# Kernel optimization log

Hardware: AMD Instinct MI355X
Metric: run time of the kernel (lower is better)

## Reference

```python
import jax, jax.numpy as jnp
import numpy as np

D_MODEL = 1024
N_HEADS = 16
HEAD_DIM = D_MODEL // N_HEADS
D_FF = 4096
LN_EPS = 1e-5


def _layer_norm(x, gamma, beta):
    mu = jnp.mean(x, axis=-1, keepdims=True)
    var = jnp.var(x, axis=-1, keepdims=True)
    return (x - mu) * jax.lax.rsqrt(var + LN_EPS) * gamma + beta


def setup_inputs() -> dict:
    key = jax.random.key(0)
    ks = jax.random.split(key, 16)
    s = 1.0 / np.sqrt(D_MODEL)
    sf = 1.0 / np.sqrt(D_FF)
    return {
        "x": jax.random.normal(ks[0], (4, 2048, D_MODEL), dtype=jnp.float32),
        "w_q": jax.random.uniform(ks[1], (D_MODEL, D_MODEL), jnp.float32, -s, s),
        "b_q": jax.random.uniform(ks[2], (D_MODEL,), jnp.float32, -s, s),
        "w_k": jax.random.uniform(ks[3], (D_MODEL, D_MODEL), jnp.float32, -s, s),
        "b_k": jax.random.uniform(ks[4], (D_MODEL,), jnp.float32, -s, s),
        "w_v": jax.random.uniform(ks[5], (D_MODEL, D_MODEL), jnp.float32, -s, s),
        "b_v": jax.random.uniform(ks[6], (D_MODEL,), jnp.float32, -s, s),
        "w_o": jax.random.uniform(ks[7], (D_MODEL, D_MODEL), jnp.float32, -s, s),
        "b_o": jax.random.uniform(ks[8], (D_MODEL,), jnp.float32, -s, s),
        "ln1_g": jnp.ones((D_MODEL,), jnp.float32),
        "ln1_b": jnp.zeros((D_MODEL,), jnp.float32),
        "w1": jax.random.uniform(ks[9], (D_MODEL, D_FF), jnp.float32, -s, s),
        "b1": jax.random.uniform(ks[10], (D_FF,), jnp.float32, -s, s),
        "w2": jax.random.uniform(ks[11], (D_FF, D_MODEL), jnp.float32, -sf, sf),
        "b2": jax.random.uniform(ks[12], (D_MODEL,), jnp.float32, -sf, sf),
        "ln2_g": jnp.ones((D_MODEL,), jnp.float32),
        "ln2_b": jnp.zeros((D_MODEL,), jnp.float32),
    }


def reference(x, w_q, b_q, w_k, b_k, w_v, b_v, w_o, b_o,
              ln1_g, ln1_b, w1, b1, w2, b2, ln2_g, ln2_b):
    B, S, D = x.shape
    # projections -> [B, H, S, Hd]
    def split_heads(t):
        return t.reshape(B, S, N_HEADS, HEAD_DIM).transpose(0, 2, 1, 3)
    q = split_heads(x @ w_q + b_q)
    k = split_heads(x @ w_k + b_k)
    v = split_heads(x @ w_v + b_v)
    scale = jnp.float32(np.sqrt(HEAD_DIM))
    scores = jnp.einsum('bhqd,bhkd->bhqk', q, k) / scale
    attn = jax.nn.softmax(scores, axis=-1)  # dropout = identity in eval
    ctx = jnp.einsum('bhqk,bhkd->bhqd', attn, v)
    ctx = ctx.transpose(0, 2, 1, 3).reshape(B, S, D)
    attn_out = ctx @ w_o + b_o
    h = _layer_norm(x + attn_out, ln1_g, ln1_b)
    ffn = jax.nn.relu(h @ w1 + b1) @ w2 + b2
    return _layer_norm(h + ffn, ln2_g, ln2_b)
```

## Files before the change

kernel.cpp:

```cpp
#include <hip/hip_runtime.h>
#include <cstdint>
#include <cstddef>

typedef unsigned short u16;
typedef short s16x8 __attribute__((ext_vector_type(8)));
typedef unsigned short u16x8 __attribute__((ext_vector_type(8)));
typedef unsigned short u16x4 __attribute__((ext_vector_type(4)));
typedef float f32x4 __attribute__((ext_vector_type(4)));

#define MFMA_BF16(a, b, c) __builtin_amdgcn_mfma_f32_16x16x32_bf16((a), (b), (c), 0, 0, 0)

__device__ __forceinline__ float b2f(u16 u) {
    union { unsigned int i; float f; } x;
    x.i = ((unsigned int)u) << 16;
    return x.f;
}
__device__ __forceinline__ u16 f2b(float f) {
    union { float f; unsigned int i; } x;
    x.f = f;
    return (u16)((x.i + 0x8000u) >> 16);
}
__device__ __forceinline__ float exp2_hw(float x) {
    float r;
    asm volatile("v_exp_f32 %0, %1" : "=v"(r) : "v"(x));
    return r;
}

__device__ __forceinline__ void gload_lds16(const u16* g, u16* l) {
    __builtin_amdgcn_global_load_lds((__attribute__((address_space(1))) void*)(g),
                                     (__attribute__((address_space(3))) void*)(l),
                                     16, 0, 0);
}

__global__ __launch_bounds__(256)
void cvt_f32_bf16(const float* __restrict__ in, u16* __restrict__ out) {
    const int i = (blockIdx.x * 256 + threadIdx.x) * 8;
    float4 a = *(const float4*)(in + i);
    float4 b = *(const float4*)(in + i + 4);
    u16x8 o;
    o[0] = f2b(a.x); o[1] = f2b(a.y); o[2] = f2b(a.z); o[3] = f2b(a.w);
    o[4] = f2b(b.x); o[5] = f2b(b.y); o[6] = f2b(b.z); o[7] = f2b(b.w);
    *(u16x8*)(out + i) = o;
}

__global__ __launch_bounds__(256)
void transpose_cvt(const float* __restrict__ in, u16* __restrict__ out, int R, int C) {
    __shared__ u16 t[64][68];
    const int tc = blockIdx.x * 64, tr = blockIdx.y * 64;
    for (int i = 0; i < 16; i++) {
        int idx = threadIdx.x + i * 256;
        int r = idx >> 6, c = idx & 63;
        t[r][c] = f2b(in[(size_t)(tr + r) * C + tc + c]);
    }
    __syncthreads();
    for (int i = 0; i < 16; i++) {
        int idx = threadIdx.x + i * 256;
        int r = idx >> 6, c = idx & 63;
        out[(size_t)(tc + r) * R + tr + c] = t[c][r];
    }
}

enum { EPI_PLAIN = 0, EPI_RELU = 1, EPI_QKV = 2 };
#define SC_QK 0.1803368801111204f

template <int EPI>
__global__ __launch_bounds__(256)
void gemm_bt(const u16* __restrict__ A, const u16* __restrict__ Bt,
             const float* __restrict__ bias0, const float* __restrict__ bias1,
             const float* __restrict__ bias2,
             u16* __restrict__ C0, u16* __restrict__ C1, u16* __restrict__ C2,
             int M, int N, int K) {
    __shared__ u16 As[128 * 32];
    __shared__ u16 Bs[128 * 32];
    const int tid = threadIdx.x;
    const int lane = tid & 63;
    const int wave = tid >> 6;
    const int qd = lane >> 4, cl = lane & 15;
    const int wr = (wave >> 1) * 64, wc = (wave & 1) * 64;
    const int m0 = blockIdx.x * 128, n0 = blockIdx.y * 128;

    const int eo0 = tid * 8, eo1 = 2048 + tid * 8;
    const u16* Ag0 = A + (size_t)(m0 + (eo0 >> 5)) * K + (eo0 & 31);
    const u16* Ag1 = A + (size_t)(m0 + (eo1 >> 5)) * K + (eo1 & 31);
    const u16* Bg0 = Bt + (size_t)(n0 + (eo0 >> 5)) * K + (eo0 & 31);
    const u16* Bg1 = Bt + (size_t)(n0 + (eo1 >> 5)) * K + (eo1 & 31);

    const f32x4 Z = {0.f, 0.f, 0.f, 0.f};
    f32x4 acc[4][4];
    for (int i = 0; i < 4; i++)
        for (int j = 0; j < 4; j++) acc[i][j] = Z;

    for (int k = 0; k < K; k += 32) {
        __syncthreads();
        gload_lds16(Ag0 + k, As + eo0);
        gload_lds16(Ag1 + k, As + eo1);
        gload_lds16(Bg0 + k, Bs + eo0);
        gload_lds16(Bg1 + k, Bs + eo1);
        __syncthreads();
        s16x8 af[4], bfr[4];
        for (int i = 0; i < 4; i++)
            af[i] = *(const s16x8*)(As + (wr + i * 16 + cl) * 32 + qd * 8);
        for (int j = 0; j < 4; j++)
            bfr[j] = *(const s16x8*)(Bs + (wc + j * 16 + cl) * 32 + qd * 8);
        for (int i = 0; i < 4; i++)
            for (int j = 0; j < 4; j++)
                acc[i][j] = MFMA_BF16(af[i], bfr[j], acc[i][j]);
    }

    for (int j = 0; j < 4; j++) {
        const int col = n0 + wc + j * 16 + cl;
        float bv;
        if (EPI == EPI_QKV) {
            const int t = col >> 10, nn = col & 1023;
            const float* bp = (t == 0) ? bias0 : ((t == 1) ? bias1 : bias2);
            bv = bp[nn];
        } else {
            bv = bias0[col];
        }
        if (EPI == EPI_QKV && (col >> 10) == 2) {
            const int nn = col & 1023;
            const int hh = nn >> 6, d = nn & 63;
            for (int i = 0; i < 4; i++) {
                const int row0 = m0 + wr + i * 16 + qd * 4;
                const int b = row0 >> 11, s = row0 & 2047;
                const int bh = b * 16 + hh;
                u16x4 pk;
                for (int r = 0; r < 4; r++) pk[r] = f2b(acc[i][j][r] + bv);
                *(u16x4*)(&C2[((size_t)bh * 64 + d) * 2048 + s]) = pk;
            }
        } else {
            for (int i = 0; i < 4; i++) {
                for (int r = 0; r < 4; r++) {
                    const int row = m0 + wr + i * 16 + qd * 4 + r;
                    float v = acc[i][j][r] + bv;
                    if (EPI == EPI_RELU) v = fmaxf(v, 0.f);
                    if (EPI == EPI_QKV) {
                        const int t = col >> 10, nn = col & 1023;
                        const int hh = nn >> 6, d = nn & 63;
                        const int b = row >> 11, s = row & 2047;
                        const int bh = b * 16 + hh;
                        if (t == 0)
                            C0[((size_t)bh * 2048 + s) * 64 + d] = f2b(v * SC_QK);
                        else
                            C1[((size_t)bh * 2048 + s) * 64 + d] = f2b(v);
                    } else {
                        C0[(size_t)row * N + col] = f2b(v);
                    }
                }
            }
        }
    }
}

__global__ __launch_bounds__(256)
void flash_attn(const u16* __restrict__ Q, const u16* __restrict__ K,
                const u16* __restrict__ Vt, u16* __restrict__ ctx) {
    __shared__ u16 Ks[64 * 64];
    __shared__ u16 Vs[64 * 64];
    __shared__ u16 Ps[4][32 * 72];
    const int tid = threadIdx.x, lane = tid & 63, wave = tid >> 6;
    const int qd = lane >> 4, cl = lane & 15;
    const int bh = blockIdx.y;
    const int s0 = blockIdx.x * 128 + wave * 32;

    const u16* Qb = Q + ((size_t)bh * 2048 + s0) * 64;
    s16x8 qf[2][2];
    for (int m = 0; m < 2; m++) {
        qf[m][0] = *(const s16x8*)(Qb + (m * 16 + cl) * 64 + qd * 8);
        qf[m][1] = *(const s16x8*)(Qb + (m * 16 + cl) * 64 + 32 + qd * 8);
    }

    const f32x4 Z = {0.f, 0.f, 0.f, 0.f};
    f32x4 o_acc[2][4], l_lane[2];
    for (int m = 0; m < 2; m++) {
        l_lane[m] = Z;
        for (int t = 0; t < 4; t++) o_acc[m][t] = Z;
    }

    const u16* Kb = K + (size_t)bh * 2048 * 64;
    const u16* Vb = Vt + (size_t)bh * 64 * 2048;

    const int e0 = tid, e1 = tid + 256;
    const int r0 = e0 >> 3, bb0 = (e0 & 7) ^ (r0 & 7);
    const int r1 = e1 >> 3, bb1 = (e1 & 7) ^ (r1 & 7);
    u16* pw = &Ps[wave][0];

    for (int kb = 0; kb < 32; kb++) {
        __syncthreads();
        gload_lds16(Kb + (size_t)(kb * 64 + r0) * 64 + bb0 * 8, Ks + e0 * 8);
        gload_lds16(Kb + (size_t)(kb * 64 + r1) * 64 + bb1 * 8, Ks + e1 * 8);
        gload_lds16(Vb + (size_t)r0 * 2048 + kb * 64 + bb0 * 8, Vs + e0 * 8);
        gload_lds16(Vb + (size_t)r1 * 2048 + kb * 64 + bb1 * 8, Vs + e1 * 8);
        __syncthreads();

        f32x4 sacc[2][4];
        for (int m = 0; m < 2; m++)
            for (int t = 0; t < 4; t++) sacc[m][t] = Z;
        for (int t = 0; t < 4; t++) {
            const int row = t * 16 + cl;
            s16x8 kf0 = *(const s16x8*)(Ks + row * 64 + (qd ^ (row & 7)) * 8);
            s16x8 kf1 = *(const s16x8*)(Ks + row * 64 + ((qd + 4) ^ (row & 7)) * 8);
            for (int m = 0; m < 2; m++) {
                sacc[m][t] = MFMA_BF16(qf[m][0], kf0, sacc[m][t]);
                sacc[m][t] = MFMA_BF16(qf[m][1], kf1, sacc[m][t]);
            }
        }

        for (int m = 0; m < 2; m++)
            for (int t = 0; t < 4; t++) {
                f32x4 p;
                for (int r = 0; r < 4; r++) p[r] = exp2_hw(sacc[m][t][r]);
                l_lane[m] += p;
                for (int r = 0; r < 4; r++)
                    pw[(m * 16 + qd * 4 + r) * 72 + t * 16 + cl] = f2b(p[r]);
            }

        for (int kk = 0; kk < 2; kk++) {
            s16x8 vf[4];
            for (int t = 0; t < 4; t++) {
                const int row = t * 16 + cl;
                vf[t] = *(const s16x8*)(Vs + row * 64 +
                                        ((kk * 4 + qd) ^ (row & 7)) * 8);
            }
            for (int m = 0; m < 2; m++) {
                s16x8 pf = *(const s16x8*)(pw + (m * 16 + cl) * 72 + kk * 32 + qd * 8);
                for (int t = 0; t < 4; t++)
                    o_acc[m][t] = MFMA_BF16(pf, vf[t], o_acc[m][t]);
            }
        }
    }

    const int b = bh >> 4, hh = bh & 15;
    for (int m = 0; m < 2; m++)
        for (int r = 0; r < 4; r++) {
            float l = l_lane[m][r];
            for (int off = 1; off < 16; off <<= 1)
                l += __shfl_xor(l, off, 16);
            const float inv = 1.f / l;
            const int s = s0 + m * 16 + qd * 4 + r;
            for (int t = 0; t < 4; t++)
                ctx[((size_t)(b * 2048 + s)) * 1024 + hh * 64 + t * 16 + cl] =
                    f2b(o_acc[m][t][r] * inv);
        }
}

template <int MODE>
__global__ __launch_bounds__(256)
void ln_res(const void* __restrict__ Xv, const u16* __restrict__ Y,
            const float* __restrict__ G, const float* __restrict__ Bp,
            void* __restrict__ Ov) {
    const int row = blockIdx.x * 4 + (threadIdx.x >> 6);
    const int lane = threadIdx.x & 63;
    const int off = lane * 16;
    float v[16];
    float s = 0.f, s2 = 0.f;
    const u16* y = Y + (size_t)row * 1024 + off;
    if (MODE == 0) {
        const float* X = (const float*)Xv + (size_t)row * 1024 + off;
        for (int i = 0; i < 2; i++) {
            float4 xa = *(const float4*)(X + i * 8);
            float4 xb = *(const float4*)(X + i * 8 + 4);
            u16x8 yv = *(const u16x8*)(y + i * 8);
            float xs[8] = {xa.x, xa.y, xa.z, xa.w, xb.x, xb.y, xb.z, xb.w};
            for (int j = 0; j < 8; j++) {
                const float t = xs[j] + b2f(yv[j]);
                v[i * 8 + j] = t;
                s += t;
                s2 += t * t;
            }
        }
    } else {
        const u16* X = (const u16*)Xv + (size_t)row * 1024 + off;
        for (int i = 0; i < 2; i++) {
            u16x8 xv = *(const u16x8*)(X + i * 8);
            u16x8 yv = *(const u16x8*)(y + i * 8);
            for (int j = 0; j < 8; j++) {
                const float t = b2f(xv[j]) + b2f(yv[j]);
                v[i * 8 + j] = t;
                s += t;
                s2 += t * t;
            }
        }
    }
    for (int o = 32; o >= 1; o >>= 1) {
        s += __shfl_xor(s, o, 64);
        s2 += __shfl_xor(s2, o, 64);
    }
    const float mu = s * (1.f / 1024.f);
    const float var = s2 * (1.f / 1024.f) - mu * mu;
    const float rs = rsqrtf(var + 1e-5f);
    const float* g = G + off;
    const float* bp = Bp + off;
    for (int i = 0; i < 2; i++) {
        float4 ga = *(const float4*)(g + i * 8);
        float4 gb = *(const float4*)(g + i * 8 + 4);
        float4 ba = *(const float4*)(bp + i * 8);
        float4 bb = *(const float4*)(bp + i * 8 + 4);
        float gs[8] = {ga.x, ga.y, ga.z, ga.w, gb.x, gb.y, gb.z, gb.w};
        float bs[8] = {ba.x, ba.y, ba.z, ba.w, bb.x, bb.y, bb.z, bb.w};
        if (MODE == 0) {
            u16* o = (u16*)Ov + (size_t)row * 1024 + off;
            u16x8 ov;
            for (int j = 0; j < 8; j++)
                ov[j] = f2b((v[i * 8 + j] - mu) * rs * gs[j] + bs[j]);
            *(u16x8*)(o + i * 8) = ov;
        } else {
            float* o = (float*)Ov + (size_t)row * 1024 + off;
            float4 o0, o1;
            o0.x = (v[i * 8 + 0] - mu) * rs * gs[0] + bs[0];
            o0.y = (v[i * 8 + 1] - mu) * rs * gs[1] + bs[1];
            o0.z = (v[i * 8 + 2] - mu) * rs * gs[2] + bs[2];
            o0.w = (v[i * 8 + 3] - mu) * rs * gs[3] + bs[3];
            o1.x = (v[i * 8 + 4] - mu) * rs * gs[4] + bs[4];
            o1.y = (v[i * 8 + 5] - mu) * rs * gs[5] + bs[5];
            o1.z = (v[i * 8 + 6] - mu) * rs * gs[6] + bs[6];
            o1.w = (v[i * 8 + 7] - mu) * rs * gs[7] + bs[7];
            *(float4*)(o + i * 8) = o0;
            *(float4*)(o + i * 8 + 4) = o1;
        }
    }
}

extern "C" void kernel_launch(void* const* d_in, const int* in_sizes, int n_in,
                              void* d_out, int out_size, void* d_ws, size_t ws_size,
                              hipStream_t stream) {
    const float* x    = (const float*)d_in[0];
    const float* w_q  = (const float*)d_in[1];
    const float* b_q  = (const float*)d_in[2];
    const float* w_k  = (const float*)d_in[3];
    const float* b_k  = (const float*)d_in[4];
    const float* w_v  = (const float*)d_in[5];
    const float* b_v  = (const float*)d_in[6];
    const float* w_o  = (const float*)d_in[7];
    const float* b_o  = (const float*)d_in[8];
    const float* ln1g = (const float*)d_in[9];
    const float* ln1b = (const float*)d_in[10];
    const float* w1   = (const float*)d_in[11];
    const float* b1   = (const float*)d_in[12];
    const float* w2   = (const float*)d_in[13];
    const float* b2   = (const float*)d_in[14];
    const float* ln2g = (const float*)d_in[15];
    const float* ln2b = (const float*)d_in[16];
    float* out = (float*)d_out;

    char* ws = (char*)d_ws;
    const size_t MB = 1024 * 1024;
    u16* wqkv_t = (u16*)(ws + 0);
    u16* wo_t   = (u16*)(ws + 6 * MB);
    u16* w1_t   = (u16*)(ws + 8 * MB);
    u16* w2_t   = (u16*)(ws + 16 * MB);
    u16* x_bf   = (u16*)(ws + 24 * MB);
    u16* Qs     = (u16*)(ws + 40 * MB);
    u16* Kk     = (u16*)(ws + 56 * MB);
    u16* Vt     = (u16*)(ws + 72 * MB);
    u16* ctx    = (u16*)(ws + 88 * MB);
    u16* attn   = (u16*)(ws + 104 * MB);
    u16* h      = attn;
    u16* ffn1   = (u16*)(ws + 24 * MB);
    u16* ffn2   = (u16*)(ws + 88 * MB);

    transpose_cvt<<<dim3(16, 16), 256, 0, stream>>>(w_q, wqkv_t, 1024, 1024);
    transpose_cvt<<<dim3(16, 16), 256, 0, stream>>>(w_k, wqkv_t + 1024 * 1024, 1024, 1024);
    transpose_cvt<<<dim3(16, 16), 256, 0, stream>>>(w_v, wqkv_t + 2 * 1024 * 1024, 1024, 1024);
    transpose_cvt<<<dim3(16, 16), 256, 0, stream>>>(w_o, wo_t, 1024, 1024);
    transpose_cvt<<<dim3(64, 16), 256, 0, stream>>>(w1, w1_t, 1024, 4096);
    transpose_cvt<<<dim3(16, 64), 256, 0, stream>>>(w2, w2_t, 4096, 1024);

    cvt_f32_bf16<<<4096, 256, 0, stream>>>(x, x_bf);

    gemm_bt<EPI_QKV><<<dim3(64, 24), 256, 0, stream>>>(
        x_bf, wqkv_t, b_q, b_k, b_v, Qs, Kk, Vt, 8192, 3072, 1024);

    flash_attn<<<dim3(16, 64), 256, 0, stream>>>(Qs, Kk, Vt, ctx);

    gemm_bt<EPI_PLAIN><<<dim3(64, 8), 256, 0, stream>>>(
        ctx, wo_t, b_o, nullptr, nullptr, attn, nullptr, nullptr, 8192, 1024, 1024);

    ln_res<0><<<2048, 256, 0, stream>>>(x, attn, ln1g, ln1b, h);

    gemm_bt<EPI_RELU><<<dim3(64, 32), 256, 0, stream>>>(
        h, w1_t, b1, nullptr, nullptr, ffn1, nullptr, nullptr, 8192, 4096, 1024);
    gemm_bt<EPI_PLAIN><<<dim3(64, 8), 256, 0, stream>>>(
        ffn1, w2_t, b2, nullptr, nullptr, ffn2, nullptr, nullptr, 8192, 1024, 4096);

    ln_res<1><<<2048, 256, 0, stream>>>(h, ffn2, ln2g, ln2b, out);

    (void)in_sizes; (void)n_in; (void)out_size; (void)ws_size;
}
```

Baseline: 580.8 us.

## Deepen GEMM K-tile to 64 with swizzled LDS; load attention K/V directly to registers

The GEMM now stages a 64-wide K slice per iteration into an XOR-swizzled LDS tile, which halves the number of barrier pairs per output tile and avoids bank conflicts on the fragment reads. The flash attention kernel drops its shared K/V staging and block barriers. Each wave loads its K and V fragments straight from global memory into registers, and the V loads are issued early so they overlap the softmax. In exchange the four waves of a block each fetch the same K/V data on their own, relying on cache for reuse, and register pressure rises.

New measurement: 671.5 us. +15.6%, slower.

```diff
diff --git a/kernel.cpp b/kernel.cpp
--- a/kernel.cpp
+++ b/kernel.cpp
@@ -70,8 +70,8 @@
              const float* __restrict__ bias2,
              u16* __restrict__ C0, u16* __restrict__ C1, u16* __restrict__ C2,
              int M, int N, int K) {
-    __shared__ u16 As[128 * 32];
-    __shared__ u16 Bs[128 * 32];
+    __shared__ u16 As[128 * 64];
+    __shared__ u16 Bs[128 * 64];
     const int tid = threadIdx.x;
     const int lane = tid & 63;
     const int wave = tid >> 6;
@@ -79,32 +79,46 @@
     const int wr = (wave >> 1) * 64, wc = (wave & 1) * 64;
     const int m0 = blockIdx.x * 128, n0 = blockIdx.y * 128;
 
-    const int eo0 = tid * 8, eo1 = 2048 + tid * 8;
-    const u16* Ag0 = A + (size_t)(m0 + (eo0 >> 5)) * K + (eo0 & 31);
-    const u16* Ag1 = A + (size_t)(m0 + (eo1 >> 5)) * K + (eo1 & 31);
-    const u16* Bg0 = Bt + (size_t)(n0 + (eo0 >> 5)) * K + (eo0 & 31);
-    const u16* Bg1 = Bt + (size_t)(n0 + (eo1 >> 5)) * K + (eo1 & 31);
+    const u16* AgP[4];
+    const u16* BgP[4];
+    int dsto[4];
+    for (int c = 0; c < 4; c++) {
+        const int d = tid * 8 + c * 2048;
+        const int row = d >> 6;
+        const int sblk = ((d >> 3) & 7) ^ (row & 7);
+        AgP[c] = A + (size_t)(m0 + row) * K + sblk * 8;
+        BgP[c] = Bt + (size_t)(n0 + row) * K + sblk * 8;
+        dsto[c] = d;
+    }
 
     const f32x4 Z = {0.f, 0.f, 0.f, 0.f};
     f32x4 acc[4][4];
     for (int i = 0; i < 4; i++)
         for (int j = 0; j < 4; j++) acc[i][j] = Z;
 
-    for (int k = 0; k < K; k += 32) {
+    for (int k = 0; k < K; k += 64) {
         __syncthreads();
-        gload_lds16(Ag0 + k, As + eo0);
-        gload_lds16(Ag1 + k, As + eo1);
-        gload_lds16(Bg0 + k, Bs + eo0);
-        gload_lds16(Bg1 + k, Bs + eo1);
+        for (int c = 0; c < 4; c++) {
+            gload_lds16(AgP[c] + k, As + dsto[c]);
+            gload_lds16(BgP[c] + k, Bs + dsto[c]);
+        }
         __syncthreads();
-        s16x8 af[4], bfr[4];
-        for (int i = 0; i < 4; i++)
-            af[i] = *(const s16x8*)(As + (wr + i * 16 + cl) * 32 + qd * 8);
-        for (int j = 0; j < 4; j++)
-            bfr[j] = *(const s16x8*)(Bs + (wc + j * 16 + cl) * 32 + qd * 8);
-        for (int i = 0; i < 4; i++)
-            for (int j = 0; j < 4; j++)
-                acc[i][j] = MFMA_BF16(af[i], bfr[j], acc[i][j]);
+        for (int kk = 0; kk < 2; kk++) {
+            s16x8 af[4], bfr[4];
+            for (int i = 0; i < 4; i++) {
+                const int row = wr + i * 16 + cl;
+                af[i] = *(const s16x8*)(As + row * 64 +
+                                        (((kk << 2) | qd) ^ (row & 7)) * 8);
+            }
+            for (int j = 0; j < 4; j++) {
+                const int row = wc + j * 16 + cl;
+                bfr[j] = *(const s16x8*)(Bs + row * 64 +
+                                         (((kk << 2) | qd) ^ (row & 7)) * 8);
+            }
+            for (int i = 0; i < 4; i++)
+                for (int j = 0; j < 4; j++)
+                    acc[i][j] = MFMA_BF16(af[i], bfr[j], acc[i][j]);
+        }
     }
 
     for (int j = 0; j < 4; j++) {
@@ -155,8 +169,6 @@
 __global__ __launch_bounds__(256)
 void flash_attn(const u16* __restrict__ Q, const u16* __restrict__ K,
                 const u16* __restrict__ Vt, u16* __restrict__ ctx) {
-    __shared__ u16 Ks[64 * 64];
-    __shared__ u16 Vs[64 * 64];
     __shared__ u16 Ps[4][32 * 72];
     const int tid = threadIdx.x, lane = tid & 63, wave = tid >> 6;
     const int qd = lane >> 4, cl = lane & 15;
@@ -179,32 +191,30 @@
 
     const u16* Kb = K + (size_t)bh * 2048 * 64;
     const u16* Vb = Vt + (size_t)bh * 64 * 2048;
-
-    const int e0 = tid, e1 = tid + 256;
-    const int r0 = e0 >> 3, bb0 = (e0 & 7) ^ (r0 & 7);
-    const int r1 = e1 >> 3, bb1 = (e1 & 7) ^ (r1 & 7);
     u16* pw = &Ps[wave][0];
 
     for (int kb = 0; kb < 32; kb++) {
-        __syncthreads();
-        gload_lds16(Kb + (size_t)(kb * 64 + r0) * 64 + bb0 * 8, Ks + e0 * 8);
-        gload_lds16(Kb + (size_t)(kb * 64 + r1) * 64 + bb1 * 8, Ks + e1 * 8);
-        gload_lds16(Vb + (size_t)r0 * 2048 + kb * 64 + bb0 * 8, Vs + e0 * 8);
-        gload_lds16(Vb + (size_t)r1 * 2048 + kb * 64 + bb1 * 8, Vs + e1 * 8);
-        __syncthreads();
+        s16x8 kf[4][2];
+        for (int t = 0; t < 4; t++) {
+            const u16* kr = Kb + (size_t)(kb * 64 + t * 16 + cl) * 64;
+            kf[t][0] = *(const s16x8*)(kr + qd * 8);
+            kf[t][1] = *(const s16x8*)(kr + 32 + qd * 8);
+        }
 
         f32x4 sacc[2][4];
         for (int m = 0; m < 2; m++)
             for (int t = 0; t < 4; t++) sacc[m][t] = Z;
-        for (int t = 0; t < 4; t++) {
-            const int row = t * 16 + cl;
-            s16x8 kf0 = *(const s16x8*)(Ks + row * 64 + (qd ^ (row & 7)) * 8);
-            s16x8 kf1 = *(const s16x8*)(Ks + row * 64 + ((qd + 4) ^ (row & 7)) * 8);
+        for (int t = 0; t < 4; t++)
             for (int m = 0; m < 2; m++) {
-                sacc[m][t] = MFMA_BF16(qf[m][0], kf0, sacc[m][t]);
-                sacc[m][t] = MFMA_BF16(qf[m][1], kf1, sacc[m][t]);
-            }
-        }
+                sacc[m][t] = MFMA_BF16(qf[m][0], kf[t][0], sacc[m][t]);
+                sacc[m][t] = MFMA_BF16(qf[m][1], kf[t][1], sacc[m][t]);
+            }
+
+        s16x8 vf[2][4];
+        for (int kk = 0; kk < 2; kk++)
+            for (int t = 0; t < 4; t++)
+                vf[kk][t] = *(const s16x8*)(Vb + (size_t)(t * 16 + cl) * 2048 +
+                                            kb * 64 + kk * 32 + qd * 8);
 
         for (int m = 0; m < 2; m++)
             for (int t = 0; t < 4; t++) {
@@ -215,19 +225,12 @@
                     pw[(m * 16 + qd * 4 + r) * 72 + t * 16 + cl] = f2b(p[r]);
             }
 
-        for (int kk = 0; kk < 2; kk++) {
-            s16x8 vf[4];
-            for (int t = 0; t < 4; t++) {
-                const int row = t * 16 + cl;
-                vf[t] = *(const s16x8*)(Vs + row * 64 +
-                                        ((kk * 4 + qd) ^ (row & 7)) * 8);
-            }
+        for (int kk = 0; kk < 2; kk++)
             for (int m = 0; m < 2; m++) {
                 s16x8 pf = *(const s16x8*)(pw + (m * 16 + cl) * 72 + kk * 32 + qd * 8);
                 for (int t = 0; t < 4; t++)
-                    o_acc[m][t] = MFMA_BF16(pf, vf[t], o_acc[m][t]);
-            }
-        }
+                    o_acc[m][t] = MFMA_BF16(pf, vf[kk][t], o_acc[m][t]);
+            }
     }
 
     const int b = bh >> 4, hh = bh & 15;
```
